# Optimization experiments

Measured on AMD Instinct MI355X. Metric: run time of the kernel, lower is better.

Reference implementation:

```python
import jax, jax.numpy as jnp
import numpy as np
from jax import lax

B, T, K = 512, 1024, 48


def setup_inputs() -> dict:
    key = jax.random.key(0)
    k1, k2, k3, k4, k5, k6 = jax.random.split(key, 6)
    emissions = jax.random.normal(k1, (B, T, K), dtype=jnp.float32)
    lengths = jax.random.randint(k2, (B,), 1, T + 1)  # every seq has >=1 valid step
    raw_tags = jax.random.randint(k3, (B, T), 0, K)
    pos = jnp.arange(T)[None, :]
    tags = jnp.where(pos < lengths[:, None], raw_tags, -1)  # -1 = pad, as in pad_sequence
    u = lambda k, s: jax.random.uniform(k, s, minval=-0.1, maxval=0.1, dtype=jnp.float32)
    return {
        "emissions": emissions,
        "tags": tags,
        "start_transitions": u(k4, (K,)),
        "end_transitions": u(k5, (K,)),
        "transitions": u(k6, (K, K)),
    }


def _crf_loss(emissions, tags, mask, start_transitions, end_transitions, transitions):
    """-sum_b log p(tags_b | emissions_b)  (torchcrf reduction='sum')."""
    maskf = mask.astype(emissions.dtype)
    safe_tags = jnp.where(mask, tags, 0)
    b_idx = jnp.arange(emissions.shape[0])

    # ---- numerator: score of the gold path ----
    emit_scores = jnp.take_along_axis(emissions, safe_tags[:, :, None], axis=2)[..., 0]  # [B,T]
    trans_scores = transitions[safe_tags[:, :-1], safe_tags[:, 1:]]  # [B,T-1]
    score = start_transitions[safe_tags[:, 0]] + emit_scores[:, 0]
    score = score + jnp.sum((trans_scores + emit_scores[:, 1:]) * maskf[:, 1:], axis=1)
    lengths = mask.sum(axis=1)
    last_tags = safe_tags[b_idx, lengths - 1]
    score = score + end_transitions[last_tags]

    # ---- denominator: log partition via forward algorithm (scan over time) ----
    em_t = jnp.transpose(emissions, (1, 0, 2))  # [T,B,K]
    mk_t = jnp.transpose(mask, (1, 0))          # [T,B]

    def step(alpha, xm):
        e, m = xm  # e:[B,K], m:[B]
        nxt = jax.nn.logsumexp(alpha[:, :, None] + transitions[None], axis=1) + e
        return jnp.where(m[:, None], nxt, alpha), None

    alpha0 = start_transitions[None, :] + em_t[0]
    alpha, _ = lax.scan(step, alpha0, (em_t[1:], mk_t[1:]))
    log_z = jax.nn.logsumexp(alpha + end_transitions[None, :], axis=1)
    return -jnp.sum(score - log_z)


def _viterbi(emissions, mask, start_transitions, end_transitions, transitions):
    em_t = jnp.transpose(emissions, (1, 0, 2))  # [T,B,K]
    mk_t = jnp.transpose(mask, (1, 0))          # [T,B]
    ident = jnp.arange(K, dtype=jnp.int32)[None, :]  # identity backpointer for padded steps

    def vstep(alpha, xm):
        e, m = xm
        scores = alpha[:, :, None] + transitions[None]  # [B,K(prev),K(cur)]
        best_prev = jnp.argmax(scores, axis=1).astype(jnp.int32)  # [B,K]
        nxt = jnp.max(scores, axis=1) + e
        alpha2 = jnp.where(m[:, None], nxt, alpha)
        bp = jnp.where(m[:, None], best_prev, ident)
        return alpha2, bp

    alpha0 = start_transitions[None, :] + em_t[0]
    alpha, bps = lax.scan(vstep, alpha0, (em_t[1:], mk_t[1:]))  # bps: [T-1,B,K]
    best_last = jnp.argmax(alpha + end_transitions[None, :], axis=1).astype(jnp.int32)  # [B]

    def btstep(cur, bp):
        prev = jnp.take_along_axis(bp, cur[:, None], axis=1)[:, 0]
        return prev, cur

    first_tag, rest = lax.scan(btstep, best_last, bps, reverse=True)  # rest[t] = tag at t+1
    best_tags = jnp.concatenate([first_tag[None], rest], axis=0).T  # [B,T]
    return jnp.where(mask, best_tags, -1)


def reference(emissions, tags, start_transitions, end_transitions, transitions):
    mask = tags > -1
    loss = _crf_loss(emissions, tags, mask, start_transitions, end_transitions, transitions)
    pred_tags = _viterbi(emissions, mask, start_transitions, end_transitions, transitions)
    return loss, pred_tags
```

## Files before the change

### kernel.cpp

```cpp
#include <hip/hip_runtime.h>

#define BB 512
#define TT 1024
#define KK 48
#define NINF (-1e30f)

__device__ __forceinline__ float rlane(float v, int l) {
    return __int_as_float(__builtin_amdgcn_readlane(__float_as_int(v), l));
}
__device__ __forceinline__ float rfirst(float v) {
    return __int_as_float(__builtin_amdgcn_readfirstlane(__float_as_int(v)));
}

__global__ __launch_bounds__(128, 1) void crf_main(
    const float* __restrict__ em,
    const int*   __restrict__ tags,
    const float* __restrict__ st,
    const float* __restrict__ en,
    const float* __restrict__ tr,
    float* __restrict__ out,
    float* __restrict__ ws)
{
    __shared__ unsigned char s_bp[TT * KK];
    __shared__ unsigned char s_path[TT];

    const int b    = blockIdx.x;
    const int tid  = threadIdx.x;
    const int lane = tid & 63;
    const int wid  = tid >> 6;

    const float* emb = em + (size_t)b * TT * KK;
    const int*   tgb = tags + (size_t)b * TT;

    int cnt = 0;
    for (int t = lane; t < TT; t += 64) cnt += (tgb[t] > -1) ? 1 : 0;
#pragma unroll
    for (int off = 32; off >= 1; off >>= 1) cnt += __shfl_xor(cnt, off);
    const int len = cnt;

    const bool act = lane < KK;
    const int  jj  = act ? lane : (KK - 1);

    const int S = len - 1;

    if (wid == 0) {
        float sc = 0.f;
        for (int t = lane; t < len; t += 64) {
            int tg = tgb[t];
            sc += emb[t * KK + tg];
            if (t > 0) sc += tr[tgb[t - 1] * KK + tg];
        }
#pragma unroll
        for (int off = 32; off >= 1; off >>= 1) sc += __shfl_xor(sc, off);
        const float score = sc + st[tgb[0]] + en[tgb[len - 1]];

        float eTc[KK];
#pragma unroll
        for (int i = 0; i < KK; ++i) eTc[i] = __expf(tr[i * KK + jj]);

        float a0 = st[jj] + emb[jj];
        float C  = rfirst(a0);
        float p  = __expf(a0 - C);

        float e[2];
        {
            int t1 = (1 < len) ? 1 : (len - 1);
            int t2 = (2 < len) ? 2 : (len - 1);
            e[1] = emb[(size_t)t1 * KK + jj];
            e[0] = emb[(size_t)t2 * KK + jj];
        }

#define FSTEP(t_, RENORM) {                                                  \
        const float eS = e[(t_) & 1];                                        \
        float z0 = 0.f, z1 = 0.f, z2 = 0.f, z3 = 0.f;                        \
        float z4 = 0.f, z5 = 0.f, z6 = 0.f, z7 = 0.f;                        \
        _Pragma("unroll")                                                    \
        for (int q = 0; q < 6; ++q) {                                        \
            z0 = fmaf(rlane(p, 8 * q + 0), eTc[8 * q + 0], z0);              \
            z1 = fmaf(rlane(p, 8 * q + 1), eTc[8 * q + 1], z1);              \
            z2 = fmaf(rlane(p, 8 * q + 2), eTc[8 * q + 2], z2);              \
            z3 = fmaf(rlane(p, 8 * q + 3), eTc[8 * q + 3], z3);              \
            z4 = fmaf(rlane(p, 8 * q + 4), eTc[8 * q + 4], z4);              \
            z5 = fmaf(rlane(p, 8 * q + 5), eTc[8 * q + 5], z5);              \
            z6 = fmaf(rlane(p, 8 * q + 6), eTc[8 * q + 6], z6);              \
            z7 = fmaf(rlane(p, 8 * q + 7), eTc[8 * q + 7], z7);              \
        }                                                                    \
        p = (((z0 + z1) + (z2 + z3)) + ((z4 + z5) + (z6 + z7)))              \
            * __expf(eS);                                                    \
        if (RENORM) {                                                        \
            float m = rfirst(p);                                             \
            p *= __frcp_rn(m);                                               \
            C += __logf(m);                                                  \
        }                                                                    \
        int tn = (t_) + 2; tn = (tn < len) ? tn : (len - 1);                 \
        e[(t_) & 1] = emb[(size_t)tn * KK + jj];                             \
    }

        {
            int t = 1;
            for (; t + 4 <= S + 1; t += 4) {
                FSTEP(t, 0) FSTEP(t + 1, 0) FSTEP(t + 2, 0) FSTEP(t + 3, 1)
            }
            for (; t <= S; ++t) FSTEP(t, 1)
        }
#undef FSTEP

        float y = act ? (p * __expf(en[jj])) : 0.f;
#pragma unroll
        for (int off = 32; off >= 1; off >>= 1) y += __shfl_xor(y, off);
        float logz = C + __logf(y);
        if (lane == 0) ws[b] = score - logz;
    } else {
        float Tc[KK];
#pragma unroll
        for (int i = 0; i < KK; ++i) Tc[i] = tr[i * KK + jj];

        float av = st[jj] + emb[jj];

        float e[2];
        {
            int t1 = (1 < len) ? 1 : (len - 1);
            int t2 = (2 < len) ? 2 : (len - 1);
            e[1] = emb[(size_t)t1 * KK + jj];
            e[0] = emb[(size_t)t2 * KK + jj];
        }

        float xA[KK], xB[KK];
        float MA = 0.f, MB = 0.f;

#define MAXPHASE(X, MV, t_) {                                                \
        const float eS = e[(t_) & 1];                                        \
        _Pragma("unroll")                                                    \
        for (int i = 0; i < KK; ++i) X[i] = rlane(av, i) + Tc[i];            \
        float l1[16];                                                        \
        _Pragma("unroll")                                                    \
        for (int q = 0; q < 16; ++q)                                         \
            l1[q] = fmaxf(fmaxf(X[3 * q], X[3 * q + 1]), X[3 * q + 2]);      \
        float l2[6];                                                         \
        _Pragma("unroll")                                                    \
        for (int q = 0; q < 5; ++q)                                          \
            l2[q] = fmaxf(fmaxf(l1[3 * q], l1[3 * q + 1]), l1[3 * q + 2]);   \
        l2[5] = l1[15];                                                      \
        MV = fmaxf(fmaxf(fmaxf(l2[0], l2[1]), l2[2]),                        \
                   fmaxf(fmaxf(l2[3], l2[4]), l2[5]));                       \
        av = MV + eS;                                                        \
        int tn = (t_) + 2; tn = (tn < len) ? tn : (len - 1);                 \
        e[(t_) & 1] = emb[(size_t)tn * KK + jj];                             \
    }

#define ARGPHASE(X, MV, t_) {                                                \
        int a0 = 255, a1 = 255, a2 = 255, a3 = 255;                          \
        _Pragma("unroll")                                                    \
        for (int i = 11; i >= 0; --i) {                                      \
            a0 = (X[i]      == MV) ? (i)      : a0;                          \
            a1 = (X[i + 12] == MV) ? (i + 12) : a1;                          \
            a2 = (X[i + 24] == MV) ? (i + 24) : a2;                          \
            a3 = (X[i + 36] == MV) ? (i + 36) : a3;                          \
        }                                                                    \
        int bi = min(min(a0, a1), min(a2, a3));                              \
        s_bp[(t_) * KK + jj] = (unsigned char)bi;    \
    }

        if (S >= 1) {
            int t = 1;
            MAXPHASE(xA, MA, 1)
            while (t + 2 <= S) {
                MAXPHASE(xB, MB, t + 1)
                ARGPHASE(xA, MA, t)
                MAXPHASE(xA, MA, t + 2)
                ARGPHASE(xB, MB, t + 1)
                t += 2;
            }
            if (t + 1 <= S) {
                MAXPHASE(xB, MB, t + 1)
                ARGPHASE(xA, MA, t)
                ARGPHASE(xB, MB, t + 1)
            } else {
                ARGPHASE(xA, MA, t)
            }
        }
#undef MAXPHASE
#undef ARGPHASE

        float v = act ? (av + en[jj]) : NINF;
        float M = v;
#pragma unroll
        for (int off = 32; off >= 1; off >>= 1) M = fmaxf(M, __shfl_xor(M, off));
        unsigned long long msk = __ballot(v == M);
        int cur = __ffsll(msk) - 1;
        s_path[len - 1] = (unsigned char)cur;

        int t = len - 1;
        while (t >= 1) {
            const int n = (t < 8) ? t : 8;
            unsigned r[8];
#pragma unroll
            for (int k = 0; k < 8; ++k)
                r[k] = (k < n) ? (unsigned)s_bp[(t - k) * KK + jj] : 0u;
#pragma unroll
            for (int k = 0; k < 8; ++k) {
                if (k < n) {
                    cur = __builtin_amdgcn_readlane((int)r[k], cur);
                    if (lane == 0) s_path[t - k - 1] = (unsigned char)cur;
                }
            }
            t -= n;
        }

        float* ob = out + 1 + (size_t)b * TT;
        for (int tt = lane; tt < TT; tt += 64)
            ob[tt] = (tt < len) ? (float)s_path[tt] : -1.0f;
    }
}

__global__ __launch_bounds__(512) void loss_reduce(const float* __restrict__ ws,
                                                   float* __restrict__ out)
{
    __shared__ float sh[8];
    const int lane = threadIdx.x & 63;
    const int w    = threadIdx.x >> 6;
    float s = ws[threadIdx.x];
#pragma unroll
    for (int off = 32; off >= 1; off >>= 1) s += __shfl_xor(s, off);
    if (lane == 0) sh[w] = s;
    __syncthreads();
    if (threadIdx.x == 0) {
        float tot = 0.f;
        for (int i = 0; i < 8; ++i) tot += sh[i];
        out[0] = -tot;
    }
}

extern "C" void kernel_launch(void* const* d_in, const int* in_sizes, int n_in,
                              void* d_out, int out_size, void* d_ws, size_t ws_size,
                              hipStream_t stream)
{
    const float* em   = (const float*)d_in[0];
    const int*   tags = (const int*)d_in[1];
    const float* st   = (const float*)d_in[2];
    const float* en   = (const float*)d_in[3];
    const float* tr   = (const float*)d_in[4];
    float* out = (float*)d_out;
    float* wsf = (float*)d_ws;

    hipLaunchKernelGGL(crf_main, dim3(BB), dim3(128), 0, stream,
                       em, tags, st, en, tr, out, wsf);
    hipLaunchKernelGGL(loss_reduce, dim3(1), dim3(512), 0, stream, wsf, out);
}
```

Measured before the change: 534.8 us.

## Broadcast recurrence state via LDS float4 reads and use bit-packed argmin

The forward and Viterbi recurrences no longer broadcast per-lane state with 48 readlane instructions per step. Each wave now writes its state vector to a small shared-memory buffer and reads it back as float4 broadcast loads. The Viterbi argmax is also rewritten: each difference from the max is packed with its index into an unsigned value and reduced with a min tree, replacing the chained compare-select. The goal is fewer scalar-transfer instructions and shorter dependency chains, at the cost of an LDS write-then-read round trip on the serial critical path of every time step.

```diff
diff --git a/kernel.cpp b/kernel.cpp
--- a/kernel.cpp
+++ b/kernel.cpp
@@ -5,9 +5,6 @@
 #define KK 48
 #define NINF (-1e30f)
 
-__device__ __forceinline__ float rlane(float v, int l) {
-    return __int_as_float(__builtin_amdgcn_readlane(__float_as_int(v), l));
-}
 __device__ __forceinline__ float rfirst(float v) {
     return __int_as_float(__builtin_amdgcn_readfirstlane(__float_as_int(v)));
 }
@@ -23,6 +20,7 @@
 {
     __shared__ unsigned char s_bp[TT * KK];
     __shared__ unsigned char s_path[TT];
+    __shared__ float s_avb[2][64];
 
     const int b    = blockIdx.x;
     const int tid  = threadIdx.x;
@@ -62,6 +60,8 @@
         float C  = rfirst(a0);
         float p  = __expf(a0 - C);
 
+        const float4* S4 = (const float4*)(&s_avb[0][0]);
+
         float e[2];
         {
             int t1 = (1 < len) ? 1 : (len - 1);
@@ -72,18 +72,20 @@
 
 #define FSTEP(t_, RENORM) {                                                  \
         const float eS = e[(t_) & 1];                                        \
+        s_avb[0][lane] = p;              \
         float z0 = 0.f, z1 = 0.f, z2 = 0.f, z3 = 0.f;                        \
         float z4 = 0.f, z5 = 0.f, z6 = 0.f, z7 = 0.f;                        \
         _Pragma("unroll")                                                    \
         for (int q = 0; q < 6; ++q) {                                        \
-            z0 = fmaf(rlane(p, 8 * q + 0), eTc[8 * q + 0], z0);              \
-            z1 = fmaf(rlane(p, 8 * q + 1), eTc[8 * q + 1], z1);              \
-            z2 = fmaf(rlane(p, 8 * q + 2), eTc[8 * q + 2], z2);              \
-            z3 = fmaf(rlane(p, 8 * q + 3), eTc[8 * q + 3], z3);              \
-            z4 = fmaf(rlane(p, 8 * q + 4), eTc[8 * q + 4], z4);              \
-            z5 = fmaf(rlane(p, 8 * q + 5), eTc[8 * q + 5], z5);              \
-            z6 = fmaf(rlane(p, 8 * q + 6), eTc[8 * q + 6], z6);              \
-            z7 = fmaf(rlane(p, 8 * q + 7), eTc[8 * q + 7], z7);              \
+            float4 v0 = S4[2 * q], v1 = S4[2 * q + 1];                       \
+            z0 = fmaf(v0.x, eTc[8 * q + 0], z0);                             \
+            z1 = fmaf(v0.y, eTc[8 * q + 1], z1);                             \
+            z2 = fmaf(v0.z, eTc[8 * q + 2], z2);                             \
+            z3 = fmaf(v0.w, eTc[8 * q + 3], z3);                             \
+            z4 = fmaf(v1.x, eTc[8 * q + 4], z4);                             \
+            z5 = fmaf(v1.y, eTc[8 * q + 5], z5);                             \
+            z6 = fmaf(v1.z, eTc[8 * q + 6], z6);                             \
+            z7 = fmaf(v1.w, eTc[8 * q + 7], z7);                             \
         }                                                                    \
         p = (((z0 + z1) + (z2 + z3)) + ((z4 + z5) + (z6 + z7)))              \
             * __expf(eS);                                                    \
@@ -117,6 +119,8 @@
 
         float av = st[jj] + emb[jj];
 
+        const float4* S4 = (const float4*)(&s_avb[1][0]);
+
         float e[2];
         {
             int t1 = (1 < len) ? 1 : (len - 1);
@@ -130,8 +134,15 @@
 
 #define MAXPHASE(X, MV, t_) {                                                \
         const float eS = e[(t_) & 1];                                        \
-        _Pragma("unroll")                                                    \
-        for (int i = 0; i < KK; ++i) X[i] = rlane(av, i) + Tc[i];            \
+        s_avb[1][lane] = av;             \
+        _Pragma("unroll")                                                    \
+        for (int q = 0; q < 12; ++q) {                                       \
+            float4 v = S4[q];                                                \
+            X[4 * q + 0] = v.x + Tc[4 * q + 0];                              \
+            X[4 * q + 1] = v.y + Tc[4 * q + 1];                              \
+            X[4 * q + 2] = v.z + Tc[4 * q + 2];                              \
+            X[4 * q + 3] = v.w + Tc[4 * q + 3];                              \
+        }                                                                    \
         float l1[16];                                                        \
         _Pragma("unroll")                                                    \
         for (int q = 0; q < 16; ++q)                                         \
@@ -149,15 +160,21 @@
     }
 
 #define ARGPHASE(X, MV, t_) {                                                \
-        int a0 = 255, a1 = 255, a2 = 255, a3 = 255;                          \
-        _Pragma("unroll")                                                    \
-        for (int i = 11; i >= 0; --i) {                                      \
-            a0 = (X[i]      == MV) ? (i)      : a0;                          \
-            a1 = (X[i + 12] == MV) ? (i + 12) : a1;                          \
-            a2 = (X[i + 24] == MV) ? (i + 24) : a2;                          \
-            a3 = (X[i + 36] == MV) ? (i + 36) : a3;                          \
-        }                                                                    \
-        int bi = min(min(a0, a1), min(a2, a3));                              \
+        unsigned u[KK];                                                      \
+        _Pragma("unroll")                                                    \
+        for (int i = 0; i < KK; ++i)                                         \
+            u[i] = (unsigned)__float_as_int(X[i] - MV) | (unsigned)i;        \
+        unsigned m1[16];                                                     \
+        _Pragma("unroll")                                                    \
+        for (int q = 0; q < 16; ++q)                                         \
+            m1[q] = min(min(u[3 * q], u[3 * q + 1]), u[3 * q + 2]);          \
+        unsigned m2[6];                                                      \
+        _Pragma("unroll")                                                    \
+        for (int q = 0; q < 5; ++q)                                          \
+            m2[q] = min(min(m1[3 * q], m1[3 * q + 1]), m1[3 * q + 2]);       \
+        m2[5] = m1[15];                                                      \
+        unsigned bi = min(min(min(m2[0], m2[1]), m2[2]),                     \
+                          min(min(m2[3], m2[4]), m2[5]));                    \
         s_bp[(t_) * KK + jj] = (unsigned char)bi;    \
     }
 
```

Measured after the change: 509.1 us. 4.8% less time.

## Split Viterbi into producer max wave and two consumer argmax waves via LDS ring

Applied to the files above, without the earlier changes.

Grows each block from two to four wavefronts. One wave runs only the Viterbi max recurrence and publishes each step's alpha to a shared-memory ring buffer guarded by flags. Two extra waves read the ring on alternating timesteps and compute backpointers with a packed-key min reduction, taking argmax off the serial critical path. The forward-algorithm wave and the new waves read broadcast values through LDS float4 loads instead of per-lane readlane. This adds spin-wait synchronization, higher register and LDS pressure, and relies on volatile shared-memory ordering between waves being correct.

```diff
diff --git a/kernel.cpp b/kernel.cpp
--- a/kernel.cpp
+++ b/kernel.cpp
@@ -3,26 +3,70 @@
 #define BB 512
 #define TT 1024
 #define KK 48
+#define RING 16
 #define NINF (-1e30f)
 
-__device__ __forceinline__ float rlane(float v, int l) {
-    return __int_as_float(__builtin_amdgcn_readlane(__float_as_int(v), l));
-}
+#define CLOBBER() asm volatile("" ::: "memory")
+
 __device__ __forceinline__ float rfirst(float v) {
     return __int_as_float(__builtin_amdgcn_readfirstlane(__float_as_int(v)));
 }
 
-__global__ __launch_bounds__(128, 1) void crf_main(
-    const float* __restrict__ em,
-    const int*   __restrict__ tags,
-    const float* __restrict__ st,
-    const float* __restrict__ en,
-    const float* __restrict__ tr,
-    float* __restrict__ out,
-    float* __restrict__ ws)
+#define MAXTREE(X, MV) {                                                     \
+        float l1[16];                                                        \
+        _Pragma("unroll")                                                    \
+        for (int q_ = 0; q_ < 16; ++q_)                                      \
+            l1[q_] = fmaxf(fmaxf(X[3 * q_], X[3 * q_ + 1]), X[3 * q_ + 2]);  \
+        float l2[6];                                                         \
+        _Pragma("unroll")                                                    \
+        for (int q_ = 0; q_ < 5; ++q_)                                       \
+            l2[q_] = fmaxf(fmaxf(l1[3 * q_], l1[3 * q_ + 1]),                \
+                           l1[3 * q_ + 2]);                                  \
+        l2[5] = l1[15];                                                      \
+        MV = fmaxf(fmaxf(fmaxf(l2[0], l2[1]), l2[2]),                        \
+                   fmaxf(fmaxf(l2[3], l2[4]), l2[5]));                       \
+    }
+
+#define XADDS(R4, X) {                                                       \
+        _Pragma("unroll")                                                    \
+        for (int q_ = 0; q_ < 12; ++q_) {                                    \
+            float4 v_ = R4[q_];                                              \
+            X[4 * q_ + 0] = v_.x + Tc[4 * q_ + 0];                           \
+            X[4 * q_ + 1] = v_.y + Tc[4 * q_ + 1];                           \
+            X[4 * q_ + 2] = v_.z + Tc[4 * q_ + 2];                           \
+            X[4 * q_ + 3] = v_.w + Tc[4 * q_ + 3];                           \
+        }                                                                    \
+    }
+
+#define ARGKEY(X, MV, BI) {                                                  \
+        unsigned u[KK];                                                      \
+        _Pragma("unroll")                                                    \
+        for (int i_ = 0; i_ < KK; ++i_)                                      \
+            u[i_] = (unsigned)__float_as_int(X[i_] - MV) | (unsigned)i_;     \
+        unsigned m1[16];                                                     \
+        _Pragma("unroll")                                                    \
+        for (int q_ = 0; q_ < 16; ++q_)                                      \
+            m1[q_] = min(min(u[3 * q_], u[3 * q_ + 1]), u[3 * q_ + 2]);      \
+        unsigned m2[6];                                                      \
+        _Pragma("unroll")                                                    \
+        for (int q_ = 0; q_ < 5; ++q_)                                       \
+            m2[q_] = min(min(m1[3 * q_], m1[3 * q_ + 1]), m1[3 * q_ + 2]);   \
+        m2[5] = m1[15];                                                      \
+        BI = min(min(min(m2[0], m2[1]), m2[2]),                              \
+                 min(min(m2[3], m2[4]), m2[5]));                             \
+    }
+
+__global__ __launch_bounds__(256, 2) void crf_pc(
+    const float* __restrict__ em, const int* __restrict__ tags,
+    const float* __restrict__ st, const float* __restrict__ en,
+    const float* __restrict__ tr, float* __restrict__ out,
+    float* __restrict__ wsl)
 {
     __shared__ unsigned char s_bp[TT * KK];
     __shared__ unsigned char s_path[TT];
+    __shared__ __align__(16) float s_ring[RING][64];
+    __shared__ __align__(16) float s_favb[64];
+    __shared__ int s_flag, s_c0, s_c1;
 
     const int b    = blockIdx.x;
     const int tid  = threadIdx.x;
@@ -32,6 +76,8 @@
     const float* emb = em + (size_t)b * TT * KK;
     const int*   tgb = tags + (size_t)b * TT;
 
+    if (tid == 0) { s_flag = -1; s_c0 = 0; s_c1 = 0; }
+
     int cnt = 0;
     for (int t = lane; t < TT; t += 64) cnt += (tgb[t] > -1) ? 1 : 0;
 #pragma unroll
@@ -40,8 +86,11 @@
 
     const bool act = lane < KK;
     const int  jj  = act ? lane : (KK - 1);
-
-    const int S = len - 1;
+    const int  S   = len - 1;
+
+    __syncthreads();
+
+    float av_final = NINF;
 
     if (wid == 0) {
         float sc = 0.f;
@@ -62,6 +111,8 @@
         float C  = rfirst(a0);
         float p  = __expf(a0 - C);
 
+        const float4* S4 = (const float4*)(&s_favb[0]);
+
         float e[2];
         {
             int t1 = (1 < len) ? 1 : (len - 1);
@@ -72,30 +123,31 @@
 
 #define FSTEP(t_, RENORM) {                                                  \
         const float eS = e[(t_) & 1];                                        \
+        s_favb[lane] = p;                       \
         float z0 = 0.f, z1 = 0.f, z2 = 0.f, z3 = 0.f;                        \
         float z4 = 0.f, z5 = 0.f, z6 = 0.f, z7 = 0.f;                        \
         _Pragma("unroll")                                                    \
-        for (int q = 0; q < 6; ++q) {                                        \
-            z0 = fmaf(rlane(p, 8 * q + 0), eTc[8 * q + 0], z0);              \
-            z1 = fmaf(rlane(p, 8 * q + 1), eTc[8 * q + 1], z1);              \
-            z2 = fmaf(rlane(p, 8 * q + 2), eTc[8 * q + 2], z2);              \
-            z3 = fmaf(rlane(p, 8 * q + 3), eTc[8 * q + 3], z3);              \
-            z4 = fmaf(rlane(p, 8 * q + 4), eTc[8 * q + 4], z4);              \
-            z5 = fmaf(rlane(p, 8 * q + 5), eTc[8 * q + 5], z5);              \
-            z6 = fmaf(rlane(p, 8 * q + 6), eTc[8 * q + 6], z6);              \
-            z7 = fmaf(rlane(p, 8 * q + 7), eTc[8 * q + 7], z7);              \
+        for (int q_ = 0; q_ < 6; ++q_) {                                     \
+            float4 v0 = S4[2 * q_], v1 = S4[2 * q_ + 1];                     \
+            z0 = fmaf(v0.x, eTc[8 * q_ + 0], z0);                            \
+            z1 = fmaf(v0.y, eTc[8 * q_ + 1], z1);                            \
+            z2 = fmaf(v0.z, eTc[8 * q_ + 2], z2);                            \
+            z3 = fmaf(v0.w, eTc[8 * q_ + 3], z3);                            \
+            z4 = fmaf(v1.x, eTc[8 * q_ + 4], z4);                            \
+            z5 = fmaf(v1.y, eTc[8 * q_ + 5], z5);                            \
+            z6 = fmaf(v1.z, eTc[8 * q_ + 6], z6);                            \
+            z7 = fmaf(v1.w, eTc[8 * q_ + 7], z7);                            \
         }                                                                    \
         p = (((z0 + z1) + (z2 + z3)) + ((z4 + z5) + (z6 + z7)))              \
             * __expf(eS);                                                    \
         if (RENORM) {                                                        \
-            float m = rfirst(p);                                             \
-            p *= __frcp_rn(m);                                               \
-            C += __logf(m);                                                  \
+            float m_ = rfirst(p);                                            \
+            p *= __frcp_rn(m_);                                              \
+            C += __logf(m_);                                                 \
         }                                                                    \
         int tn = (t_) + 2; tn = (tn < len) ? tn : (len - 1);                 \
         e[(t_) & 1] = emb[(size_t)tn * KK + jj];                             \
     }
-
         {
             int t = 1;
             for (; t + 4 <= S + 1; t += 4) {
@@ -109,13 +161,19 @@
 #pragma unroll
         for (int off = 32; off >= 1; off >>= 1) y += __shfl_xor(y, off);
         float logz = C + __logf(y);
-        if (lane == 0) ws[b] = score - logz;
-    } else {
+        if (lane == 0) wsl[b] = score - logz;
+    } else if (wid == 1) {
+        __builtin_amdgcn_s_setprio(1);
         float Tc[KK];
 #pragma unroll
         for (int i = 0; i < KK; ++i) Tc[i] = tr[i * KK + jj];
 
         float av = st[jj] + emb[jj];
+
+        *(volatile float*)&s_ring[0][lane] = av;
+        CLOBBER();
+        if (lane == 0) *(volatile int*)&s_flag = 0;
+        CLOBBER();
 
         float e[2];
         {
@@ -125,64 +183,67 @@
             e[0] = emb[(size_t)t2 * KK + jj];
         }
 
-        float xA[KK], xB[KK];
-        float MA = 0.f, MB = 0.f;
-
-#define MAXPHASE(X, MV, t_) {                                                \
-        const float eS = e[(t_) & 1];                                        \
-        _Pragma("unroll")                                                    \
-        for (int i = 0; i < KK; ++i) X[i] = rlane(av, i) + Tc[i];            \
-        float l1[16];                                                        \
-        _Pragma("unroll")                                                    \
-        for (int q = 0; q < 16; ++q)                                         \
-            l1[q] = fmaxf(fmaxf(X[3 * q], X[3 * q + 1]), X[3 * q + 2]);      \
-        float l2[6];                                                         \
-        _Pragma("unroll")                                                    \
-        for (int q = 0; q < 5; ++q)                                          \
-            l2[q] = fmaxf(fmaxf(l1[3 * q], l1[3 * q + 1]), l1[3 * q + 2]);   \
-        l2[5] = l1[15];                                                      \
-        MV = fmaxf(fmaxf(fmaxf(l2[0], l2[1]), l2[2]),                        \
-                   fmaxf(fmaxf(l2[3], l2[4]), l2[5]));                       \
-        av = MV + eS;                                                        \
+#define PSTEP(t_, PAR) {                                                     \
+        const float4* R4 =                                                   \
+            (const float4*)(&s_ring[((t_) - 1) & (RING - 1)][0]);            \
+        float X[KK];                                                         \
+        XADDS(R4, X)                                                         \
+        float M; MAXTREE(X, M)                                               \
+        av = M + e[PAR];                                                     \
+        CLOBBER();                                                           \
+        *(volatile float*)&s_ring[(t_) & (RING - 1)][lane] = av;             \
+        CLOBBER();                                                           \
+        if (lane == 0) *(volatile int*)&s_flag = (t_);                       \
+        CLOBBER();                                                           \
         int tn = (t_) + 2; tn = (tn < len) ? tn : (len - 1);                 \
-        e[(t_) & 1] = emb[(size_t)tn * KK + jj];                             \
-    }
-
-#define ARGPHASE(X, MV, t_) {                                                \
-        int a0 = 255, a1 = 255, a2 = 255, a3 = 255;                          \
-        _Pragma("unroll")                                                    \
-        for (int i = 11; i >= 0; --i) {                                      \
-            a0 = (X[i]      == MV) ? (i)      : a0;                          \
-            a1 = (X[i + 12] == MV) ? (i + 12) : a1;                          \
-            a2 = (X[i + 24] == MV) ? (i + 24) : a2;                          \
-            a3 = (X[i + 36] == MV) ? (i + 36) : a3;                          \
-        }                                                                    \
-        int bi = min(min(a0, a1), min(a2, a3));                              \
-        s_bp[(t_) * KK + jj] = (unsigned char)bi;    \
-    }
-
-        if (S >= 1) {
-            int t = 1;
-            MAXPHASE(xA, MA, 1)
-            while (t + 2 <= S) {
-                MAXPHASE(xB, MB, t + 1)
-                ARGPHASE(xA, MA, t)
-                MAXPHASE(xA, MA, t + 2)
-                ARGPHASE(xB, MB, t + 1)
-                t += 2;
+        e[PAR] = emb[(size_t)tn * KK + jj];                                  \
+    }
+
+        int t = 1;
+        for (; t + 1 <= S; t += 2) {
+            if ((t & 7) == 1) {
+                while (min(*(volatile int*)&s_c0,
+                           *(volatile int*)&s_c1) < t - 8)
+                    __builtin_amdgcn_s_sleep(1);
+                CLOBBER();
             }
-            if (t + 1 <= S) {
-                MAXPHASE(xB, MB, t + 1)
-                ARGPHASE(xA, MA, t)
-                ARGPHASE(xB, MB, t + 1)
-            } else {
-                ARGPHASE(xA, MA, t)
-            }
-        }
-#undef MAXPHASE
-#undef ARGPHASE
-
-        float v = act ? (av + en[jj]) : NINF;
+            PSTEP(t, 1) PSTEP(t + 1, 0)
+        }
+        if (t <= S) PSTEP(t, 1)
+#undef PSTEP
+        __builtin_amdgcn_s_setprio(0);
+        av_final = av;
+    } else {
+        float Tc[KK];
+#pragma unroll
+        for (int i = 0; i < KK; ++i) Tc[i] = tr[i * KK + jj];
+
+        const int start = (wid == 2) ? 1 : 2;
+        volatile int* cslot = (wid == 2) ? (volatile int*)&s_c0
+                                         : (volatile int*)&s_c1;
+
+        for (int tau = start; tau <= S; tau += 2) {
+            const int want = tau - 1;
+            while (*(volatile int*)&s_flag < want)
+                __builtin_amdgcn_s_sleep(1);
+            CLOBBER();
+            const float4* R4 =
+                (const float4*)(&s_ring[(tau - 1) & (RING - 1)][0]);
+            float X[KK];
+            XADDS(R4, X)
+            float M; MAXTREE(X, M)
+            unsigned bi; ARGKEY(X, M, bi)
+            s_bp[tau * KK + jj] = (unsigned char)bi;
+            CLOBBER();
+            if (lane == 0) *cslot = tau;
+            CLOBBER();
+        }
+    }
+
+    __syncthreads();
+
+    if (wid == 1) {
+        float v = act ? (av_final + en[jj]) : NINF;
         float M = v;
 #pragma unroll
         for (int off = 32; off >= 1; off >>= 1) M = fmaxf(M, __shfl_xor(M, off));
@@ -241,9 +302,9 @@
     const float* en   = (const float*)d_in[3];
     const float* tr   = (const float*)d_in[4];
     float* out = (float*)d_out;
-    float* wsf = (float*)d_ws;
-
-    hipLaunchKernelGGL(crf_main, dim3(BB), dim3(128), 0, stream,
-                       em, tags, st, en, tr, out, wsf);
-    hipLaunchKernelGGL(loss_reduce, dim3(1), dim3(512), 0, stream, wsf, out);
+    float* wsl = (float*)d_ws;
+
+    hipLaunchKernelGGL(crf_pc, dim3(BB), dim3(256), 0, stream,
+                       em, tags, st, en, tr, out, wsl);
+    hipLaunchKernelGGL(loss_reduce, dim3(1), dim3(512), 0, stream, wsl, out);
 }
```

New measurement: 475.6 us (median of 2 runs). 11.1% less time.
